# Optimization experiments

Hardware: AMD Instinct MI355X
Metric: run time of the kernel (lower is better)

Reference implementation:

```python
import jax, jax.numpy as jnp
import numpy as np

EPS = 1e-8


def box2corners(box):
    # box: (B, N, 5) = (x, y, w, h, angle_rad) -> corners (B, N, 4, 2)
    x, y, w, h, a = (box[..., i] for i in range(5))
    xs = jnp.array([0.5, -0.5, -0.5, 0.5], box.dtype) * w[..., None]
    ys = jnp.array([0.5, 0.5, -0.5, -0.5], box.dtype) * h[..., None]
    cos, sin = jnp.cos(a)[..., None], jnp.sin(a)[..., None]
    cx = xs * cos - ys * sin + x[..., None]
    cy = xs * sin + ys * cos + y[..., None]
    return jnp.stack([cx, cy], axis=-1)


def edge_intersections(c1, c2):
    # all 4x4 edge-pair segment intersections -> pts (B,N,16,2), mask (B,N,16)
    p = c1[..., :, None, :]                                  # (B,N,4,1,2)
    r = (jnp.roll(c1, -1, axis=-2) - c1)[..., :, None, :]     # edge dirs of box1
    q = c2[..., None, :, :]                                  # (B,N,1,4,2)
    s = (jnp.roll(c2, -1, axis=-2) - c2)[..., None, :, :]     # edge dirs of box2
    qp = q - p
    rxs = r[..., 0] * s[..., 1] - r[..., 1] * s[..., 0]
    t = (qp[..., 0] * s[..., 1] - qp[..., 1] * s[..., 0]) / (rxs + EPS)
    u = (qp[..., 0] * r[..., 1] - qp[..., 1] * r[..., 0]) / (rxs + EPS)
    mask = (t > 0.) & (t < 1.) & (u > 0.) & (u < 1.)
    pts = (p + t[..., None] * r) * mask[..., None]
    B, N = c1.shape[0], c1.shape[1]
    return pts.reshape(B, N, 16, 2), mask.reshape(B, N, 16)


def box_in_box(corners1, corners2):
    # True where corners of box1 lie inside box2 -> (B,N,4)
    a = corners2[..., 0:1, :]
    b = corners2[..., 1:2, :]
    d = corners2[..., 3:4, :]
    ab, ad, am = b - a, d - a, corners1 - a
    p_ab = jnp.sum(ab * am, -1) / (jnp.sum(ab * ab, -1) + EPS)
    p_ad = jnp.sum(ad * am, -1) / (jnp.sum(ad * ad, -1) + EPS)
    tol = 1e-6
    return (p_ab > -tol) & (p_ab < 1. + tol) & (p_ad > -tol) & (p_ad < 1. + tol)


def convex_area(verts, mask):
    # shoelace area of valid vertices, sorted CCW by angle around their mean
    m = mask.astype(verts.dtype)
    nv = jnp.sum(m, axis=-1)                                          # (B,N)
    mean = jnp.sum(verts * m[..., None], axis=-2) / jnp.maximum(nv, 1.)[..., None]
    v = verts - mean[..., None, :]
    ang = jnp.where(mask, jnp.arctan2(v[..., 1], v[..., 0]), 1e9)      # invalid sort last
    order = jnp.argsort(ang, axis=-1)
    v_s = jnp.take_along_axis(v, order[..., None], axis=-2)
    m_s = jnp.take_along_axis(mask, order, axis=-1)
    v_s = jnp.where(m_s[..., None], v_s, v_s[..., 0:1, :])  # pad tail with first vertex -> zero cross terms
    v_n = jnp.roll(v_s, -1, axis=-2)
    cross = v_s[..., 0] * v_n[..., 1] - v_s[..., 1] * v_n[..., 0]
    area = 0.5 * jnp.abs(jnp.sum(cross, axis=-1))
    return jnp.where(nv >= 3., area, 0.)


def diff_iou_rotated_2d(box1, box2):
    c1, c2 = box2corners(box1), box2corners(box2)
    pts, m_int = edge_intersections(c1, c2)
    m1 = box_in_box(c1, c2)
    m2 = box_in_box(c2, c1)
    verts = jnp.concatenate([c1, c2, pts], axis=-2)    # (B,N,24,2)
    mask = jnp.concatenate([m1, m2, m_int], axis=-1)   # (B,N,24)
    inter = convex_area(verts, mask)
    area1 = box1[..., 2] * box1[..., 3]
    area2 = box2[..., 2] * box2[..., 3]
    union = area1 + area2 - inter
    return inter / (union + EPS)


def setup_inputs() -> dict:
    key = jax.random.key(0)
    k1, k2, k3 = jax.random.split(key, 3)
    B, A, W, H = 16, 3, 128, 128
    pred = jax.random.uniform(k1, (B, A, W, H, 5), dtype=jnp.float32)
    target = jax.random.uniform(k2, (B, A, W, H, 5), dtype=jnp.float32)
    pos_idx = jax.random.randint(k3, (B, A, W, H), 0, 2).astype(bool)
    return {"pred": pred, "target": target, "pos_idx": pos_idx}


def reference(pred, target, pos_idx):
    eps = 1e-7
    target = target.at[..., -1].set(jnp.deg2rad(target[..., -1] * 180. - 180.))
    pred = pred.at[..., -1].set(jnp.deg2rad(pred[..., -1]))
    bs, A, w, h = target.shape[:-1]
    ious = diff_iou_rotated_2d(pred.reshape(1, -1, 5), target.reshape(1, -1, 5))
    ious = jnp.clip(ious.reshape(bs, A, w, h), eps, 1. - eps)
    m = pos_idx.astype(ious.dtype)
    # mode == 'linear': loss = 1 - iou, mean over positive samples
    loss = jnp.sum((1. - ious) * m) / jnp.maximum(jnp.sum(m), 1.)
    return loss, ious
```

## Files before the change

### kernel.cpp

```cpp
#include <hip/hip_runtime.h>

#define FEPS 1e-8f

__device__ __forceinline__ float fastrcp(float x) {
    return __builtin_amdgcn_rcpf(x);
}

__device__ __forceinline__ float clip_span(
    float a0, float a1, float inv0, float inv1, float hw, float hh)
{
    float tA0 = ( hw - a0) * inv0;
    float tB0 = (-hw - a0) * inv0;
    float tA1 = ( hh - a1) * inv1;
    float tB1 = (-hh - a1) * inv1;
    float lo0 = fminf(tA0, tB0), hi0 = fmaxf(tA0, tB0);
    float lo1 = fminf(tA1, tB1), hi1 = fmaxf(tA1, tB1);
    float t0 = fmaxf(0.0f, fmaxf(lo0, lo1));
    float t1 = fminf(1.0f, fminf(hi0, hi1));
    return fmaxf(t1 - t0, 0.0f);
}

__device__ __forceinline__ float one_iou(
    float p0, float p1, float p2, float p3, float p4,
    float t0, float t1, float t2, float t3, float t4)
{
    const float DEG = 0.017453292519943295f;
    float aa1 = p4 * DEG;
    float aa2 = (t4 * 180.0f - 180.0f) * DEG;
    float s1 = __sinf(aa1), c1 = __cosf(aa1);
    float s2 = __sinf(aa2), c2 = __cosf(aa2);

    float dx = p0 - t0, dy = p1 - t1;
    float qx =  dx * c2 + dy * s2;
    float qy = -dx * s2 + dy * c2;
    float cw = c1 * c2 + s1 * s2;
    float sw = s1 * c2 - c1 * s2;

    float hw1 = 0.5f * p2, hh1 = 0.5f * p3;
    float hw2 = 0.5f * t2, hh2 = 0.5f * t3;
    float area1 = p2 * p3, area2 = t2 * t3;

    float e1x =  hw1 * cw, e1y = hw1 * sw;
    float f1x = -hh1 * sw, f1y = hh1 * cw;

    float qpex = qx + e1x, qpey = qy + e1y;
    float qmex = qx - e1x, qmey = qy - e1y;
    float G0x = qpex + f1x, G0y = qpey + f1y;
    float G1x = qmex + f1x, G1y = qmey + f1y;
    float G2x = qmex - f1x, G2y = qmey - f1y;
    float G3x = qpex - f1x, G3y = qpey - f1y;

    float i_ex = fastrcp(-2.0f * e1x), i_ey = fastrcp(-2.0f * e1y);
    float i_fx = fastrcp(-2.0f * f1x), i_fy = fastrcp(-2.0f * f1y);

    float halfA1 = 0.5f * area1;
    float X2 = 2.0f * (qx * e1y - qy * e1x);
    float Y2 = 2.0f * (qx * f1y - qy * f1x);
    float w0 = halfA1 - X2;
    float w1 = halfA1 - Y2;
    float w2 = halfA1 + X2;
    float w3 = halfA1 + Y2;

    float sum = 0.0f;
    sum += clip_span(G0x, G0y,  i_ex,  i_ey, hw2, hh2) * w0;
    sum += clip_span(G1x, G1y,  i_fx,  i_fy, hw2, hh2) * w1;
    sum += clip_span(G2x, G2y, -i_ex, -i_ey, hw2, hh2) * w2;
    sum += clip_span(G3x, G3y, -i_fx, -i_fy, hw2, hh2) * w3;

    float e2x = hw2 * cw, e2y = -hw2 * sw;
    float f2x = hh2 * sw, f2y =  hh2 * cw;
    float mx = -(qx * cw + qy * sw);
    float my =   qx * sw - qy * cw;
    float mpex = mx + e2x, mpey = my + e2y;
    float mmex = mx - e2x, mmey = my - e2y;
    float H0x = mpex + f2x, H0y = mpey + f2y;
    float H1x = mmex + f2x, H1y = mmey + f2y;
    float H2x = mmex - f2x, H2y = mmey - f2y;
    float H3x = mpex - f2x, H3y = mpey - f2y;

    float j_ex = fastrcp(-2.0f * e2x), j_ey = fastrcp(-2.0f * e2y);
    float j_fx = fastrcp(-2.0f * f2x), j_fy = fastrcp(-2.0f * f2y);

    float span = 0.0f;
    span += clip_span(H0x, H0y,  j_ex,  j_ey, hw1, hh1);
    span += clip_span(H1x, H1y,  j_fx,  j_fy, hw1, hh1);
    span += clip_span(H2x, H2y, -j_ex, -j_ey, hw1, hh1);
    span += clip_span(H3x, H3y, -j_fx, -j_fy, hw1, hh1);
    sum += span * (0.5f * area2);

    float inter = 0.5f * fabsf(sum);
    float uni = area1 + area2 - inter;
    float iou = inter * fastrcp(uni + FEPS);
    return fminf(fmaxf(iou, 1e-7f), 1.0f - 1e-7f);
}

__global__ __launch_bounds__(256) void riou_kernel(
    const float* __restrict__ pred, const float* __restrict__ target,
    const int* __restrict__ pos_idx, float* __restrict__ out,
    float2* __restrict__ partials, int n)
{
    int gid = blockIdx.x * blockDim.x + threadIdx.x;
    float lnum = 0.0f, lden = 0.0f;

    if (gid < n) {
        const float* p = pred + (size_t)gid * 5;
        const float* t = target + (size_t)gid * 5;
        float iou = one_iou(p[0], p[1], p[2], p[3], p[4],
                            t[0], t[1], t[2], t[3], t[4]);
        out[1 + gid] = iou;
        float m = (pos_idx[gid] != 0) ? 1.0f : 0.0f;
        lnum = (1.0f - iou) * m;
        lden = m;
    }

    #pragma unroll
    for (int off = 32; off > 0; off >>= 1) {
        lnum += __shfl_down(lnum, off);
        lden += __shfl_down(lden, off);
    }
    __shared__ float snum[4], sden[4];
    int wave = threadIdx.x >> 6, lane = threadIdx.x & 63;
    if (lane == 0) { snum[wave] = lnum; sden[wave] = lden; }
    __syncthreads();
    if (threadIdx.x == 0) {
        float bn = snum[0] + snum[1] + snum[2] + snum[3];
        float bd = sden[0] + sden[1] + sden[2] + sden[3];
        partials[blockIdx.x] = make_float2(bn, bd);
    }
}

__global__ __launch_bounds__(1024) void riou_finalize(
    const float2* __restrict__ partials, int nb, float* __restrict__ out)
{
    double num = 0.0, den = 0.0;
    for (int i = threadIdx.x; i < nb; i += 1024) {
        float2 p = partials[i];
        num += (double)p.x;
        den += (double)p.y;
    }
    #pragma unroll
    for (int off = 32; off > 0; off >>= 1) {
        num += __shfl_down(num, off);
        den += __shfl_down(den, off);
    }
    __shared__ double dn[16], dd[16];
    int wave = threadIdx.x >> 6, lane = threadIdx.x & 63;
    if (lane == 0) { dn[wave] = num; dd[wave] = den; }
    __syncthreads();
    if (threadIdx.x == 0) {
        double n2 = 0.0, d2 = 0.0;
        #pragma unroll
        for (int w = 0; w < 16; ++w) { n2 += dn[w]; d2 += dd[w]; }
        out[0] = (float)(n2 / fmax(d2, 1.0));
    }
}

extern "C" void kernel_launch(void* const* d_in, const int* in_sizes, int n_in,
                              void* d_out, int out_size, void* d_ws, size_t ws_size,
                              hipStream_t stream) {
    const float* pred   = (const float*)d_in[0];
    const float* target = (const float*)d_in[1];
    const int*   posidx = (const int*)d_in[2];
    float* out = (float*)d_out;

    int n = in_sizes[0] / 5;
    int block = 256;
    int grid = (n + block - 1) / block;
    float2* partials = (float2*)d_ws;

    riou_kernel<<<grid, block, 0, stream>>>(pred, target, posidx, out,
                                            partials, n);
    riou_finalize<<<1, 1024, 0, stream>>>(partials, grid, out);
}
```

Measured before the change: 84.22 us.

## Fuse IoU and final reduction into one cooperative grid-stride kernel

Replaces the two-kernel compute-then-finalize scheme with a single cooperative kernel of 1024 blocks that grid-strides over elements, writes per-block partials with release stores, performs a grid-wide sync, and has block 0 reduce the partials. This removes the second launch and the tiny single-block finalize pass, and lowers the number of partials from about 3000 to 1024. It adds grid-sync overhead, and the fallback path now reduces in float instead of double, which slightly changes precision.

```diff
diff --git a/kernel.cpp b/kernel.cpp
--- a/kernel.cpp
+++ b/kernel.cpp
@@ -1,4 +1,7 @@
 #include <hip/hip_runtime.h>
+#include <hip/hip_cooperative_groups.h>
+
+namespace cg = cooperative_groups;
 
 #define FEPS 1e-8f
 
@@ -94,6 +97,73 @@
     return fminf(fmaxf(iou, 1e-7f), 1.0f - 1e-7f);
 }
 
+__device__ __forceinline__ unsigned long long pack2f(float a, float b) {
+    union { float f[2]; unsigned long long u; } v;
+    v.f[0] = a; v.f[1] = b;
+    return v.u;
+}
+
+__global__ __launch_bounds__(256, 4) void riou_fused(
+    const float* __restrict__ pred, const float* __restrict__ target,
+    const int* __restrict__ pos_idx, float* __restrict__ out,
+    unsigned long long* __restrict__ partials, int n)
+{
+    int stride = gridDim.x * blockDim.x;
+    int tid = blockIdx.x * blockDim.x + threadIdx.x;
+
+    float lnum = 0.0f, lden = 0.0f;
+    for (int gid = tid; gid < n; gid += stride) {
+        const float* p = pred + (size_t)gid * 5;
+        const float* t = target + (size_t)gid * 5;
+        float iou = one_iou(p[0], p[1], p[2], p[3], p[4],
+                            t[0], t[1], t[2], t[3], t[4]);
+        out[1 + gid] = iou;
+        float m = (pos_idx[gid] != 0) ? 1.0f : 0.0f;
+        lnum += (1.0f - iou) * m;
+        lden += m;
+    }
+
+    #pragma unroll
+    for (int off = 32; off > 0; off >>= 1) {
+        lnum += __shfl_down(lnum, off);
+        lden += __shfl_down(lden, off);
+    }
+    __shared__ float snum[4], sden[4];
+    int wave = threadIdx.x >> 6, lane = threadIdx.x & 63;
+    if (lane == 0) { snum[wave] = lnum; sden[wave] = lden; }
+    __syncthreads();
+    if (threadIdx.x == 0) {
+        float bn = snum[0] + snum[1] + snum[2] + snum[3];
+        float bd = sden[0] + sden[1] + sden[2] + sden[3];
+        __hip_atomic_store(&partials[blockIdx.x], pack2f(bn, bd),
+                           __ATOMIC_RELEASE, __HIP_MEMORY_SCOPE_AGENT);
+    }
+
+    cg::this_grid().sync();
+
+    if (blockIdx.x == 0) {
+        float num = 0.0f, den = 0.0f;
+        for (int i = threadIdx.x; i < (int)gridDim.x; i += 256) {
+            unsigned long long u = __hip_atomic_load(
+                &partials[i], __ATOMIC_ACQUIRE, __HIP_MEMORY_SCOPE_AGENT);
+            union { unsigned long long u; float f[2]; } v; v.u = u;
+            num += v.f[0]; den += v.f[1];
+        }
+        #pragma unroll
+        for (int off = 32; off > 0; off >>= 1) {
+            num += __shfl_down(num, off);
+            den += __shfl_down(den, off);
+        }
+        if (lane == 0) { snum[wave] = num; sden[wave] = den; }
+        __syncthreads();
+        if (threadIdx.x == 0) {
+            float n2 = snum[0] + snum[1] + snum[2] + snum[3];
+            float d2 = sden[0] + sden[1] + sden[2] + sden[3];
+            out[0] = n2 / fmaxf(d2, 1.0f);
+        }
+    }
+}
+
 __global__ __launch_bounds__(256) void riou_kernel(
     const float* __restrict__ pred, const float* __restrict__ target,
     const int* __restrict__ pos_idx, float* __restrict__ out,
@@ -101,7 +171,6 @@
 {
     int gid = blockIdx.x * blockDim.x + threadIdx.x;
     float lnum = 0.0f, lden = 0.0f;
-
     if (gid < n) {
         const float* p = pred + (size_t)gid * 5;
         const float* t = target + (size_t)gid * 5;
@@ -112,7 +181,6 @@
         lnum = (1.0f - iou) * m;
         lden = m;
     }
-
     #pragma unroll
     for (int off = 32; off > 0; off >>= 1) {
         lnum += __shfl_down(lnum, off);
@@ -123,35 +191,33 @@
     if (lane == 0) { snum[wave] = lnum; sden[wave] = lden; }
     __syncthreads();
     if (threadIdx.x == 0) {
-        float bn = snum[0] + snum[1] + snum[2] + snum[3];
-        float bd = sden[0] + sden[1] + sden[2] + sden[3];
-        partials[blockIdx.x] = make_float2(bn, bd);
+        partials[blockIdx.x] = make_float2(snum[0]+snum[1]+snum[2]+snum[3],
+                                           sden[0]+sden[1]+sden[2]+sden[3]);
     }
 }
 
 __global__ __launch_bounds__(1024) void riou_finalize(
     const float2* __restrict__ partials, int nb, float* __restrict__ out)
 {
-    double num = 0.0, den = 0.0;
+    float num = 0.0f, den = 0.0f;
     for (int i = threadIdx.x; i < nb; i += 1024) {
         float2 p = partials[i];
-        num += (double)p.x;
-        den += (double)p.y;
+        num += p.x; den += p.y;
     }
     #pragma unroll
     for (int off = 32; off > 0; off >>= 1) {
         num += __shfl_down(num, off);
         den += __shfl_down(den, off);
     }
-    __shared__ double dn[16], dd[16];
+    __shared__ float dn[16], dd[16];
     int wave = threadIdx.x >> 6, lane = threadIdx.x & 63;
     if (lane == 0) { dn[wave] = num; dd[wave] = den; }
     __syncthreads();
     if (threadIdx.x == 0) {
-        double n2 = 0.0, d2 = 0.0;
+        float n2 = 0.0f, d2 = 0.0f;
         #pragma unroll
         for (int w = 0; w < 16; ++w) { n2 += dn[w]; d2 += dd[w]; }
-        out[0] = (float)(n2 / fmax(d2, 1.0));
+        out[0] = n2 / fmaxf(d2, 1.0f);
     }
 }
 
@@ -162,13 +228,20 @@
     const float* target = (const float*)d_in[1];
     const int*   posidx = (const int*)d_in[2];
     float* out = (float*)d_out;
-
     int n = in_sizes[0] / 5;
-    int block = 256;
-    int grid = (n + block - 1) / block;
-    float2* partials = (float2*)d_ws;
-
-    riou_kernel<<<grid, block, 0, stream>>>(pred, target, posidx, out,
-                                            partials, n);
-    riou_finalize<<<1, 1024, 0, stream>>>(partials, grid, out);
-}
+
+    unsigned long long* partials_u = (unsigned long long*)d_ws;
+    void* args[] = { (void*)&pred, (void*)&target, (void*)&posidx,
+                     (void*)&out, (void*)&partials_u, (void*)&n };
+    hipError_t err = hipLaunchCooperativeKernel(
+        (const void*)riou_fused, dim3(1024), dim3(256), args, 0, stream);
+
+    if (err != hipSuccess) {
+        int block = 256;
+        int grid = (n + block - 1) / block;
+        float2* partials = (float2*)d_ws;
+        riou_kernel<<<grid, block, 0, stream>>>(pred, target, posidx, out,
+                                                partials, n);
+        riou_finalize<<<1, 1024, 0, stream>>>(partials, grid, out);
+    }
+}
```

After: 231.4 us. 175% more time.
